# Kernel tuning notes

Measured on AMD Instinct MI355X. Metric: run time of the kernel, lower is better.

The kernel has to match this reference:

```python
import jax, jax.numpy as jnp
import numpy as np

ROPE_FREQ = 100.0

def _rope1d(tok, pos, freq):
    # tok: [B, H, N, D] (D even), pos: [B, N] int positions
    D = tok.shape[-1]
    inv_freq = 1.0 / (freq ** (jnp.arange(0, D, 2, dtype=jnp.float32) / D))  # [D/2]
    ang = pos[:, None, :, None].astype(jnp.float32) * inv_freq  # [B,1,N,D/2]
    cos = jnp.concatenate([jnp.cos(ang), jnp.cos(ang)], axis=-1).astype(tok.dtype)
    sin = jnp.concatenate([jnp.sin(ang), jnp.sin(ang)], axis=-1).astype(tok.dtype)
    x1, x2 = jnp.split(tok, 2, axis=-1)
    rot = jnp.concatenate([-x2, x1], axis=-1)  # rotate_half
    return tok * cos + rot * sin

def _rope2d(tok, pos2d, freq=ROPE_FREQ):
    # tok: [B, H, N, D]; first half of D encodes y (pos2d[...,0]), second half x (pos2d[...,1])
    y, x = jnp.split(tok, 2, axis=-1)
    y = _rope1d(y, pos2d[..., 0], freq)
    x = _rope1d(x, pos2d[..., 1], freq)
    return jnp.concatenate([y, x], axis=-1)

def setup_inputs() -> dict:
    key = jax.random.key(0)
    B, N, D, Hh = 2, 2048, 768, 12
    ks = jax.random.split(key, 8)
    x = jax.random.normal(ks[0], (B, N, D), dtype=jnp.float32)
    pos2d = jax.random.randint(ks[1], (B, N, 2), 0, 64)
    rope_mask = jax.random.randint(ks[2], (B, N), 0, 2).astype(jnp.bool_)
    s = 1.0 / np.sqrt(D)
    qkv_w = jax.random.normal(ks[3], (3 * D, D), dtype=jnp.float32) * s
    qkv_b = jnp.zeros((3 * D,), dtype=jnp.float32)
    proj_w = jax.random.normal(ks[4], (D, D), dtype=jnp.float32) * s
    proj_b = jnp.zeros((D,), dtype=jnp.float32)
    return {"x": x, "qkv_w": qkv_w, "qkv_b": qkv_b, "proj_w": proj_w,
            "proj_b": proj_b, "pos2d": pos2d, "rope_mask": rope_mask}

def reference(x, qkv_w, qkv_b, proj_w, proj_b, pos2d, rope_mask):
    B, N, C = x.shape
    num_heads = 12
    head_dim = C // num_heads
    scale = head_dim ** -0.5
    qkv = x @ qkv_w.T + qkv_b  # [B,N,3C]
    qkv = qkv.reshape(B, N, 3, num_heads, head_dim).transpose(2, 0, 3, 1, 4)
    q, k, v = qkv[0], qkv[1], qkv[2]  # each [B,H,N,hd]
    q_rope = _rope2d(q, pos2d)
    k_rope = _rope2d(k, pos2d)
    mask = rope_mask[:, None, :, None]  # [B,1,N,1]
    q = jnp.where(mask, q_rope, q)
    k = jnp.where(mask, k_rope, k)
    attn = jnp.einsum('bhqd,bhkd->bhqk', q, k) * scale
    attn = jax.nn.softmax(attn, axis=-1)
    out = jnp.einsum('bhqk,bhkd->bhqd', attn, v)
    out = out.transpose(0, 2, 1, 3).reshape(B, N, C)
    out = out @ proj_w.T + proj_b
    return out
```

## Files before the change

### kernel.cpp

```cpp
#include <hip/hip_runtime.h>
#include <stdint.h>

#define B_  2
#define N_  2048
#define C_  768
#define H_  12
#define NT  (B_*N_)
#define C3  (3*C_)

typedef _Float16 h8 __attribute__((ext_vector_type(8)));
typedef _Float16 h4 __attribute__((ext_vector_type(4)));
typedef float    f4 __attribute__((ext_vector_type(4)));
typedef float    f16x __attribute__((ext_vector_type(16)));
typedef uint32_t u4 __attribute__((ext_vector_type(4)));

__device__ __forceinline__ void gload16(const void* g, void* l) {
  __builtin_amdgcn_global_load_lds((const __attribute__((address_space(1))) void*)g,
                                   (__attribute__((address_space(3))) void*)l,
                                   16, 0, 0);
}

__device__ __forceinline__ int xcd_swz(int flat, int nwg) {
  return (flat & 7) * (nwg >> 3) + (flat >> 3);
}

__global__ __launch_bounds__(256) void cvt3(const float* __restrict__ x,
                                            const float* __restrict__ w1,
                                            const float* __restrict__ w2,
                                            _Float16* __restrict__ xo,
                                            _Float16* __restrict__ w1o,
                                            _Float16* __restrict__ w2o) {
  const int NX8  = NT*C_/8;
  const int NW18 = C3*C_/8;
  int c = blockIdx.x*256 + threadIdx.x;
  const float* s; _Float16* d; int off;
  if (c < NX8)            { s = x;  d = xo;  off = c; }
  else if (c < NX8+NW18)  { s = w1; d = w1o; off = c - NX8; }
  else                    { s = w2; d = w2o; off = c - NX8 - NW18; }
  f4 a = *(const f4*)(s + (size_t)off*8);
  f4 b = *(const f4*)(s + (size_t)off*8 + 4);
  h8 o;
#pragma unroll
  for (int j = 0; j < 4; ++j) { o[j] = (_Float16)a[j]; o[j+4] = (_Float16)b[j]; }
  *(h8*)(d + (size_t)off*8) = o;
}

template<int BM, int BN>
__global__ __launch_bounds__(256) void gemm_bt(const _Float16* __restrict__ A,
                                               const _Float16* __restrict__ W,
                                               const float* __restrict__ bias,
                                               _Float16* __restrict__ Ch,
                                               float* __restrict__ Cf,
                                               int M, int N, int K) {
  __shared__ _Float16 Alds[2][BM*32];
  __shared__ _Float16 Wlds[2][BN*32];
  const int tid = threadIdx.x, lane = tid & 63, w = tid >> 6;
  const int flat = blockIdx.y * gridDim.x + blockIdx.x;
  const int wid  = xcd_swz(flat, gridDim.x * gridDim.y);
  const int bx = wid % gridDim.x, by = wid / gridDim.x;
  const int m0 = by*BM, n0 = bx*BN;
  const int wm = w >> 1, wn = w & 1;
  const int fr = lane & 15, fq = lane >> 4;
  constexpr int MT = BM/32, NTt = BN/32;
  constexpr int AI = (BM*4)/256, WI = (BN*4)/256;

  f4 acc[MT][NTt] = {};

  const _Float16* Agp[AI];
  const _Float16* Wgp[WI];
#pragma unroll
  for (int i = 0; i < AI; ++i) { int c = i*256 + tid; Agp[i] = A + (size_t)(m0 + (c>>2))*K + (c&3)*8; }
#pragma unroll
  for (int i = 0; i < WI; ++i) { int c = i*256 + tid; Wgp[i] = W + (size_t)(n0 + (c>>2))*K + (c&3)*8; }

  auto GSTAGE = [&](int buf, int kk) {
#pragma unroll
    for (int i = 0; i < AI; ++i) gload16(Agp[i] + kk, &Alds[buf][(i*256 + w*64)*8]);
#pragma unroll
    for (int i = 0; i < WI; ++i) gload16(Wgp[i] + kk, &Wlds[buf][(i*256 + w*64)*8]);
  };

  GSTAGE(0, 0);
  int cur = 0;
  for (int kk = 0; kk < K; kk += 32) {
    __syncthreads();
    if (kk + 32 < K) GSTAGE(cur^1, kk + 32);
    h8 af[MT], wf[NTt];
#pragma unroll
    for (int mt = 0; mt < MT; ++mt)
      af[mt] = *(const h8*)&Alds[cur][(wm*(BM/2) + mt*16 + fr)*32 + fq*8];
#pragma unroll
    for (int nt = 0; nt < NTt; ++nt)
      wf[nt] = *(const h8*)&Wlds[cur][(wn*(BN/2) + nt*16 + fr)*32 + fq*8];
#pragma unroll
    for (int mt = 0; mt < MT; ++mt)
#pragma unroll
      for (int nt = 0; nt < NTt; ++nt)
        acc[mt][nt] = __builtin_amdgcn_mfma_f32_16x16x32_f16(af[mt], wf[nt], acc[mt][nt], 0, 0, 0);
    cur ^= 1;
  }

#pragma unroll
  for (int nt = 0; nt < NTt; ++nt) {
    const int col = n0 + wn*(BN/2) + nt*16 + fr;
    const float bv = bias[col];
#pragma unroll
    for (int mt = 0; mt < MT; ++mt) {
      const int row = m0 + wm*(BM/2) + mt*16 + fq*4;
#pragma unroll
      for (int j = 0; j < 4; ++j) {
        const float v = acc[mt][nt][j] + bv;
        if (Ch) Ch[(size_t)(row+j)*N + col] = (_Float16)v;
        else    Cf[(size_t)(row+j)*N + col] = v;
      }
    }
  }
}

__global__ __launch_bounds__(256) void rope_scatter(const _Float16* __restrict__ QKV,
                                                    const int* __restrict__ pos2d,
                                                    const void* __restrict__ maskraw,
                                                    _Float16* __restrict__ Q,
                                                    _Float16* __restrict__ Kd,
                                                    _Float16* __restrict__ Vt) {
  const int tid = threadIdx.x;
  __shared__ int sflags;
  if (tid == 0) sflags = 0;
  __syncthreads();
  const unsigned char* mbytes = (const unsigned char*)maskraw;
  int fl = 0;
#pragma unroll
  for (int k2 = 0; k2 < 16; ++k2) {
    unsigned char v = mbytes[tid*16 + k2];
    if (v == 0x3f) fl |= 1;
    if ((k2 & 3) && v) fl |= 2;
  }
  if (fl) atomicOr(&sflags, fl);
  __syncthreads();
  const int mode = (sflags & 1) ? 2 : ((sflags & 2) ? 1 : 0);

  const int g  = blockIdx.x*256 + tid;
  const int bh = g >> 11;
  const int n  = g & 2047;
  const int b  = bh / H_, h = bh % H_;
  const int t  = b*N_ + n;

  bool msk;
  if (mode == 1)      msk = mbytes[t] != 0;
  else if (mode == 0) msk = ((const int*)maskraw)[t] != 0;
  else                msk = ((const float*)maskraw)[t] != 0.0f;

  const float py = (float)pos2d[t*2 + 0];
  const float px = (float)pos2d[t*2 + 1];

  const float QS = 0.1803368801f;

  const _Float16* row = QKV + (size_t)t*C3 + h*64;
  h8 qv[8], kv[8], vv[8];
#pragma unroll
  for (int c = 0; c < 8; ++c) {
    qv[c] = *(const h8*)&row[c*8];
    kv[c] = *(const h8*)&row[C_   + c*8];
    vv[c] = *(const h8*)&row[2*C_ + c*8];
  }
  h8 qo[8], ko[8];
#pragma unroll
  for (int i = 0; i < 16; ++i) {
    const float invf = exp2f((float)i * -0.4152410118f);
    float sy, cy, sx, cx;
    __sincosf(py * invf, &sy, &cy);
    __sincosf(px * invf, &sx, &cx);
    {
      float a = (float)qv[i>>3][i&7], bq = (float)qv[(i+16)>>3][(i+16)&7];
      float r1 = msk ? (a*cy - bq*sy) : a;
      float r2 = msk ? (bq*cy + a*sy) : bq;
      qo[i>>3][i&7]           = (_Float16)(r1 * QS);
      qo[(i+16)>>3][(i+16)&7] = (_Float16)(r2 * QS);
      float ak = (float)kv[i>>3][i&7], bk = (float)kv[(i+16)>>3][(i+16)&7];
      float s1 = msk ? (ak*cy - bk*sy) : ak;
      float s2 = msk ? (bk*cy + ak*sy) : bk;
      ko[i>>3][i&7]           = (_Float16)s1;
      ko[(i+16)>>3][(i+16)&7] = (_Float16)s2;
    }
    {
      float a = (float)qv[(i+32)>>3][(i+32)&7], bq = (float)qv[(i+48)>>3][(i+48)&7];
      float r1 = msk ? (a*cx - bq*sx) : a;
      float r2 = msk ? (bq*cx + a*sx) : bq;
      qo[(i+32)>>3][(i+32)&7] = (_Float16)(r1 * QS);
      qo[(i+48)>>3][(i+48)&7] = (_Float16)(r2 * QS);
      float ak = (float)kv[(i+32)>>3][(i+32)&7], bk = (float)kv[(i+48)>>3][(i+48)&7];
      float s1 = msk ? (ak*cx - bk*sx) : ak;
      float s2 = msk ? (bk*cx + ak*sx) : bk;
      ko[(i+32)>>3][(i+32)&7] = (_Float16)s1;
      ko[(i+48)>>3][(i+48)&7] = (_Float16)s2;
    }
  }
  _Float16* Qrow = Q  + ((size_t)bh*N_ + n)*64;
  _Float16* Krow = Kd + ((size_t)bh*N_ + n)*64;
#pragma unroll
  for (int c = 0; c < 8; ++c) { *(h8*)&Qrow[c*8] = qo[c]; *(h8*)&Krow[c*8] = ko[c]; }
  _Float16* Vb = Vt + (size_t)bh*64*N_ + n;
#pragma unroll
  for (int d = 0; d < 64; ++d) Vb[(size_t)d*N_] = vv[d>>3][d&7];
}

#define KSPLIT 2
__global__ __launch_bounds__(256, 3) void attn(const _Float16* __restrict__ Q,
                                               const _Float16* __restrict__ K,
                                               const _Float16* __restrict__ Vt,
                                               _Float16* __restrict__ Opart,
                                               float* __restrict__ lpart) {
  __shared__ _Float16 Klds[2][64*64];
  __shared__ _Float16 Vlds[2][64*64];
  const int tid = threadIdx.x, lane = tid & 63, w = tid >> 6;
  const int q32 = lane & 31;
  const int hi  = lane >> 5;
  const int flat = blockIdx.x + gridDim.x*(blockIdx.y + gridDim.y*blockIdx.z);
  const int wid  = xcd_swz(flat, 16*24*KSPLIT);
  const int qi = wid & 15;
  const int bh = (wid >> 4) % 24;
  const int z  = wid / (16*24);
  const int q0 = qi * 128;
  const int kb0 = z * (N_/KSPLIT), kb1 = kb0 + N_/KSPLIT;
  const _Float16* Qb = Q  + (size_t)bh*N_*64;
  const _Float16* Kb = K  + (size_t)bh*N_*64;
  const _Float16* Vb = Vt + (size_t)bh*64*N_;

  h8 qf[4];
#pragma unroll
  for (int s = 0; s < 4; ++s)
    qf[s] = *(const h8*)&Qb[(size_t)(q0 + w*32 + q32)*64 + s*16 + hi*8];

  f16x o2[2][2];
#pragma unroll
  for (int par = 0; par < 2; ++par)
#pragma unroll
    for (int dg = 0; dg < 2; ++dg)
#pragma unroll
      for (int r = 0; r < 16; ++r) o2[par][dg][r] = 0.f;
  float l_r = 0.f;

  const int sr_l = lane >> 3;
  const int scsw = ((lane & 7) ^ sr_l) * 8;
#define STAGE(buf, kb)                                                          \
  {                                                                             \
    _Float16* kl = &Klds[buf][(w*64)*8];                                        \
    _Float16* vl = &Vlds[buf][(w*64)*8];                                        \
    int r0 = w*8 + sr_l;                                                        \
    gload16(Kb + (size_t)((kb) + r0)*64 + scsw,      kl);                       \
    gload16(Vb + (size_t)r0*N_ + (kb) + scsw,        vl);                       \
    gload16(Kb + (size_t)((kb) + 32 + r0)*64 + scsw, kl + 256*8);               \
    gload16(Vb + (size_t)(32 + r0)*N_ + (kb) + scsw, vl + 256*8);               \
  }

  STAGE(0, kb0);
  int cur = 0;
  const int xr = (q32 & 7) << 3;

  for (int kb = kb0; kb < kb1; kb += 64) {
    __syncthreads();
    if (kb + 64 < kb1) STAGE(cur^1, kb + 64);

#pragma unroll
    for (int kg = 0; kg < 2; ++kg) {
      f16x st;
#pragma unroll
      for (int r = 0; r < 16; ++r) st[r] = -8.65617025f;
      __builtin_amdgcn_s_setprio(1);
#pragma unroll
      for (int s = 0; s < 4; ++s) {
        h8 kf = *(const h8*)&Klds[cur][(kg*32 + q32)*64 + ((s*16 + hi*8) ^ xr)];
        st = __builtin_amdgcn_mfma_f32_32x32x16_f16(kf, qf[s], st, 0, 0, 0);
      }
      __builtin_amdgcn_s_setprio(0);
      float p[16];
      float lacc = 0.f;
#pragma unroll
      for (int r = 0; r < 16; ++r) {
        p[r] = __builtin_amdgcn_exp2f(st[r]);
        lacc += p[r];
      }
      l_r += lacc;
      uint32_t dd[8];
#pragma unroll
      for (int m = 0; m < 8; ++m)
        dd[m] = __builtin_bit_cast(uint32_t, __builtin_amdgcn_cvt_pkrtz(p[2*m], p[2*m+1]));
#pragma unroll
      for (int s16 = 0; s16 < 2; ++s16) {
        uint32_t e0 = dd[4*s16+0], e2 = dd[4*s16+2];
        asm("v_permlane32_swap_b32 %0, %1" : "+v"(e0), "+v"(e2));
        uint32_t e1 = dd[4*s16+1], e3 = dd[4*s16+3];
        asm("v_permlane32_swap_b32 %0, %1" : "+v"(e1), "+v"(e3));
        u4 bb;
        bb[0] = e0; bb[1] = e1; bb[2] = e2; bb[3] = e3;
        h8 pb = __builtin_bit_cast(h8, bb);
        const int kcol = kg*32 + s16*16 + hi*8;
        __builtin_amdgcn_s_setprio(1);
#pragma unroll
        for (int dg = 0; dg < 2; ++dg) {
          h8 vf = *(const h8*)&Vlds[cur][(dg*32 + q32)*64 + (kcol ^ xr)];
          o2[s16][dg] = __builtin_amdgcn_mfma_f32_32x32x16_f16(vf, pb, o2[s16][dg], 0, 0, 0);
        }
        __builtin_amdgcn_s_setprio(0);
      }
    }
    cur ^= 1;
  }

  l_r += __shfl_xor(l_r, 32);

  _Float16* Ob = Opart + ((size_t)z*24 + bh)*N_*64;
  float*    lb = lpart + ((size_t)z*24 + bh)*N_;
  const int n = q0 + w*32 + q32;
  if (hi == 0) lb[n] = l_r;
#pragma unroll
  for (int dg = 0; dg < 2; ++dg)
#pragma unroll
    for (int rq = 0; rq < 4; ++rq) {
      h4 ov;
#pragma unroll
      for (int j = 0; j < 4; ++j)
        ov[j] = (_Float16)(o2[0][dg][rq*4 + j] + o2[1][dg][rq*4 + j]);
      *(h4*)&Ob[(size_t)n*64 + dg*32 + rq*8 + hi*4] = ov;
    }
}

__global__ __launch_bounds__(256) void combine(const _Float16* __restrict__ Opart,
                                               const float* __restrict__ lpart,
                                               _Float16* __restrict__ AO) {
  const int g  = blockIdx.x*256 + threadIdx.x;
  const int d8 = g & 7;
  const int n  = (g >> 3) & 2047;
  const int bh = g >> 14;
  const int b = bh / H_, h = bh % H_;
  const size_t r  = ((size_t)bh*N_ + n);
  const size_t sp = (size_t)24*N_;
  f4 osum[2] = {};
  float l = 0.f;
#pragma unroll
  for (int z = 0; z < KSPLIT; ++z) {
    h8 oz = *(const h8*)&Opart[(r + z*sp)*64 + d8*8];
#pragma unroll
    for (int j = 0; j < 4; ++j) { osum[0][j] += (float)oz[j]; osum[1][j] += (float)oz[j+4]; }
    l += lpart[r + z*sp];
  }
  const float inv = 1.0f / l;
  h8 rr;
#pragma unroll
  for (int j = 0; j < 4; ++j) {
    rr[j]   = (_Float16)(osum[0][j] * inv);
    rr[j+4] = (_Float16)(osum[1][j] * inv);
  }
  *(h8*)&AO[((size_t)b*N_ + n)*C_ + h*64 + d8*8] = rr;
}

extern "C" void kernel_launch(void* const* d_in, const int* in_sizes, int n_in,
                              void* d_out, int out_size, void* d_ws, size_t ws_size,
                              hipStream_t stream) {
  (void)in_sizes; (void)n_in; (void)out_size; (void)ws_size;
  const float* x      = (const float*)d_in[0];
  const float* qkv_w  = (const float*)d_in[1];
  const float* qkv_b  = (const float*)d_in[2];
  const float* proj_w = (const float*)d_in[3];
  const float* proj_b = (const float*)d_in[4];
  const int*   pos2d  = (const int*)d_in[5];
  const void*  rmask  = d_in[6];
  float* out = (float*)d_out;
  char* ws = (char*)d_ws;

  _Float16* Wqh   = (_Float16*)(ws + 0);
  _Float16* Wph   = (_Float16*)(ws + 3538944);
  _Float16* Kh    = (_Float16*)(ws + 4718592);
  _Float16* Vth   = (_Float16*)(ws + 11010048);
  _Float16* Xh    = (_Float16*)(ws + 17301504);
  _Float16* QKVh  = (_Float16*)(ws + 23592960);
  _Float16* Qh    = Xh;
  _Float16* Opart = (_Float16*)(ws + 42467328);
  float*    lpart = (float*)(ws + 55050240);
  _Float16* AOh   = QKVh;

  cvt3<<<2688, 256, 0, stream>>>(x, qkv_w, proj_w, Xh, Wqh, Wph);
  gemm_bt<64,128><<<dim3(C3/128, NT/64), 256, 0, stream>>>(Xh, Wqh, qkv_b, QKVh, nullptr, NT, C3, C_);
  rope_scatter<<<(B_*H_*N_)/256, 256, 0, stream>>>(QKVh, pos2d, rmask, Qh, Kh, Vth);
  attn<<<dim3(N_/128, B_*H_, KSPLIT), 256, 0, stream>>>(Qh, Kh, Vth, Opart, lpart);
  combine<<<(24*N_*8)/256, 256, 0, stream>>>(Opart, lpart, AOh);
  gemm_bt<64,64><<<dim3(C_/64, NT/64), 256, 0, stream>>>(AOh, Wph, proj_b, nullptr, out, NT, C_, C_);
}
```

Baseline: 111.6 us.

## Fuse RoPE, scaling and Q/K/V scatter into the QKV GEMM epilogue

Adds a dedicated QKV GEMM whose epilogue applies bias, 2D RoPE (masked), the Q scale, and writes Q/K in head-major layout and V transposed, replacing the separate rope_scatter kernel. This removes a full write and re-read of the fp16 QKV intermediate plus one kernel launch. In exchange, the epilogue does scalar 2-byte scattered stores and strided V-transpose writes, recomputes sincos per tile, and adds mask-detection work to every GEMM block. The workspace layout is reshuffled so Q no longer aliases Xh.

```diff
diff --git a/kernel.cpp b/kernel.cpp
--- a/kernel.cpp
+++ b/kernel.cpp
@@ -43,6 +43,125 @@
 #pragma unroll
   for (int j = 0; j < 4; ++j) { o[j] = (_Float16)a[j]; o[j+4] = (_Float16)b[j]; }
   *(h8*)(d + (size_t)off*8) = o;
+}
+
+__global__ __launch_bounds__(256) void gemm_qkv(const _Float16* __restrict__ A,
+                                                const _Float16* __restrict__ W,
+                                                const float* __restrict__ bias,
+                                                const int* __restrict__ pos2d,
+                                                const void* __restrict__ maskraw,
+                                                _Float16* __restrict__ Qd,
+                                                _Float16* __restrict__ Kd,
+                                                _Float16* __restrict__ Vtd) {
+  constexpr int BM = 64, BN = 128, K = C_;
+  __shared__ _Float16 Alds[2][BM*32];
+  __shared__ _Float16 Wlds[2][BN*32];
+  __shared__ int sflags;
+  const int tid = threadIdx.x, lane = tid & 63, w = tid >> 6;
+
+  if (tid == 0) sflags = 0;
+  __syncthreads();
+  const unsigned char* mbytes = (const unsigned char*)maskraw;
+  int fl = 0;
+#pragma unroll
+  for (int k2 = 0; k2 < 16; ++k2) {
+    unsigned char v = mbytes[tid*16 + k2];
+    if (v == 0x3f) fl |= 1;
+    if ((k2 & 3) && v) fl |= 2;
+  }
+  if (fl) atomicOr(&sflags, fl);
+
+  const int flat = blockIdx.y * gridDim.x + blockIdx.x;
+  const int wid  = xcd_swz(flat, gridDim.x * gridDim.y);
+  const int bx = wid % gridDim.x, by = wid / gridDim.x;
+  const int m0 = by*BM, n0 = bx*BN;
+  const int wm = w >> 1, wn = w & 1;
+  const int fr = lane & 15, fq = lane >> 4;
+
+  f4 acc[2][4] = {};
+
+  const _Float16* Agp = A + (size_t)(m0 + (tid>>2))*K + (tid&3)*8;
+  const _Float16* Wgp0 = W + (size_t)(n0 + (tid>>2))*K + (tid&3)*8;
+  const _Float16* Wgp1 = W + (size_t)(n0 + 64 + (tid>>2))*K + (tid&3)*8;
+
+  auto GSTAGE = [&](int buf, int kk) {
+    gload16(Agp  + kk, &Alds[buf][(w*64)*8]);
+    gload16(Wgp0 + kk, &Wlds[buf][(w*64)*8]);
+    gload16(Wgp1 + kk, &Wlds[buf][(256 + w*64)*8]);
+  };
+
+  GSTAGE(0, 0);
+  int cur = 0;
+  for (int kk = 0; kk < K; kk += 32) {
+    __syncthreads();
+    if (kk + 32 < K) GSTAGE(cur^1, kk + 32);
+    h8 af[2], wf[4];
+#pragma unroll
+    for (int mt = 0; mt < 2; ++mt)
+      af[mt] = *(const h8*)&Alds[cur][(wm*32 + mt*16 + fr)*32 + fq*8];
+#pragma unroll
+    for (int nt = 0; nt < 4; ++nt)
+      wf[nt] = *(const h8*)&Wlds[cur][(wn*64 + nt*16 + fr)*32 + fq*8];
+#pragma unroll
+    for (int mt = 0; mt < 2; ++mt)
+#pragma unroll
+      for (int nt = 0; nt < 4; ++nt)
+        acc[mt][nt] = __builtin_amdgcn_mfma_f32_16x16x32_f16(af[mt], wf[nt], acc[mt][nt], 0, 0, 0);
+    cur ^= 1;
+  }
+
+  const int cb   = (n0 >> 6) + wn;
+  const int matc = cb / 12;
+  const int h    = cb % 12;
+  const int mode = (sflags & 1) ? 2 : ((sflags & 2) ? 1 : 0);
+  float bv[4];
+#pragma unroll
+  for (int nt = 0; nt < 4; ++nt) bv[nt] = bias[cb*64 + nt*16 + fr];
+
+  if (matc < 2) {
+    const float invf = exp2f((float)fr * -0.4152410118f);
+    const float sc = (matc == 0) ? 0.1803368801f : 1.0f;
+    _Float16* base = (matc == 0) ? Qd : Kd;
+#pragma unroll
+    for (int mt = 0; mt < 2; ++mt)
+#pragma unroll
+      for (int j = 0; j < 4; ++j) {
+        const int t = m0 + wm*32 + mt*16 + fq*4 + j;
+        const int b = t >> 11, n = t & 2047;
+        bool msk;
+        if (mode == 1)      msk = mbytes[t] != 0;
+        else if (mode == 0) msk = ((const int*)maskraw)[t] != 0;
+        else                msk = ((const float*)maskraw)[t] != 0.0f;
+        const float py = (float)pos2d[t*2 + 0];
+        const float px = (float)pos2d[t*2 + 1];
+        float sy, cy, sx, cx;
+        __sincosf(py * invf, &sy, &cy);
+        __sincosf(px * invf, &sx, &cx);
+        const float a0 = acc[mt][0][j] + bv[0], a1 = acc[mt][1][j] + bv[1];
+        const float a2 = acc[mt][2][j] + bv[2], a3 = acc[mt][3][j] + bv[3];
+        const float r0 = msk ? (a0*cy - a1*sy) : a0;
+        const float r1 = msk ? (a1*cy + a0*sy) : a1;
+        const float r2 = msk ? (a2*cx - a3*sx) : a2;
+        const float r3 = msk ? (a3*cx + a2*sx) : a3;
+        _Float16* dst = base + ((size_t)(b*H_ + h)*N_ + n)*64;
+        dst[fr]      = (_Float16)(r0 * sc);
+        dst[fr + 16] = (_Float16)(r1 * sc);
+        dst[fr + 32] = (_Float16)(r2 * sc);
+        dst[fr + 48] = (_Float16)(r3 * sc);
+      }
+  } else {
+#pragma unroll
+    for (int mt = 0; mt < 2; ++mt)
+#pragma unroll
+      for (int j = 0; j < 4; ++j) {
+        const int t = m0 + wm*32 + mt*16 + fq*4 + j;
+        const int b = t >> 11, n = t & 2047;
+        _Float16* vb = Vtd + (size_t)(b*H_ + h)*64*N_ + n;
+#pragma unroll
+        for (int nt = 0; nt < 4; ++nt)
+          vb[(size_t)(nt*16 + fr)*N_] = (_Float16)(acc[mt][nt][j] + bv[nt]);
+      }
+  }
 }
 
 template<int BM, int BN>
@@ -115,93 +234,6 @@
       }
     }
   }
-}
-
-__global__ __launch_bounds__(256) void rope_scatter(const _Float16* __restrict__ QKV,
-                                                    const int* __restrict__ pos2d,
-                                                    const void* __restrict__ maskraw,
-                                                    _Float16* __restrict__ Q,
-                                                    _Float16* __restrict__ Kd,
-                                                    _Float16* __restrict__ Vt) {
-  const int tid = threadIdx.x;
-  __shared__ int sflags;
-  if (tid == 0) sflags = 0;
-  __syncthreads();
-  const unsigned char* mbytes = (const unsigned char*)maskraw;
-  int fl = 0;
-#pragma unroll
-  for (int k2 = 0; k2 < 16; ++k2) {
-    unsigned char v = mbytes[tid*16 + k2];
-    if (v == 0x3f) fl |= 1;
-    if ((k2 & 3) && v) fl |= 2;
-  }
-  if (fl) atomicOr(&sflags, fl);
-  __syncthreads();
-  const int mode = (sflags & 1) ? 2 : ((sflags & 2) ? 1 : 0);
-
-  const int g  = blockIdx.x*256 + tid;
-  const int bh = g >> 11;
-  const int n  = g & 2047;
-  const int b  = bh / H_, h = bh % H_;
-  const int t  = b*N_ + n;
-
-  bool msk;
-  if (mode == 1)      msk = mbytes[t] != 0;
-  else if (mode == 0) msk = ((const int*)maskraw)[t] != 0;
-  else                msk = ((const float*)maskraw)[t] != 0.0f;
-
-  const float py = (float)pos2d[t*2 + 0];
-  const float px = (float)pos2d[t*2 + 1];
-
-  const float QS = 0.1803368801f;
-
-  const _Float16* row = QKV + (size_t)t*C3 + h*64;
-  h8 qv[8], kv[8], vv[8];
-#pragma unroll
-  for (int c = 0; c < 8; ++c) {
-    qv[c] = *(const h8*)&row[c*8];
-    kv[c] = *(const h8*)&row[C_   + c*8];
-    vv[c] = *(const h8*)&row[2*C_ + c*8];
-  }
-  h8 qo[8], ko[8];
-#pragma unroll
-  for (int i = 0; i < 16; ++i) {
-    const float invf = exp2f((float)i * -0.4152410118f);
-    float sy, cy, sx, cx;
-    __sincosf(py * invf, &sy, &cy);
-    __sincosf(px * invf, &sx, &cx);
-    {
-      float a = (float)qv[i>>3][i&7], bq = (float)qv[(i+16)>>3][(i+16)&7];
-      float r1 = msk ? (a*cy - bq*sy) : a;
-      float r2 = msk ? (bq*cy + a*sy) : bq;
-      qo[i>>3][i&7]           = (_Float16)(r1 * QS);
-      qo[(i+16)>>3][(i+16)&7] = (_Float16)(r2 * QS);
-      float ak = (float)kv[i>>3][i&7], bk = (float)kv[(i+16)>>3][(i+16)&7];
-      float s1 = msk ? (ak*cy - bk*sy) : ak;
-      float s2 = msk ? (bk*cy + ak*sy) : bk;
-      ko[i>>3][i&7]           = (_Float16)s1;
-      ko[(i+16)>>3][(i+16)&7] = (_Float16)s2;
-    }
-    {
-      float a = (float)qv[(i+32)>>3][(i+32)&7], bq = (float)qv[(i+48)>>3][(i+48)&7];
-      float r1 = msk ? (a*cx - bq*sx) : a;
-      float r2 = msk ? (bq*cx + a*sx) : bq;
-      qo[(i+32)>>3][(i+32)&7] = (_Float16)(r1 * QS);
-      qo[(i+48)>>3][(i+48)&7] = (_Float16)(r2 * QS);
-      float ak = (float)kv[(i+32)>>3][(i+32)&7], bk = (float)kv[(i+48)>>3][(i+48)&7];
-      float s1 = msk ? (ak*cx - bk*sx) : ak;
-      float s2 = msk ? (bk*cx + ak*sx) : bk;
-      ko[(i+32)>>3][(i+32)&7] = (_Float16)s1;
-      ko[(i+48)>>3][(i+48)&7] = (_Float16)s2;
-    }
-  }
-  _Float16* Qrow = Q  + ((size_t)bh*N_ + n)*64;
-  _Float16* Krow = Kd + ((size_t)bh*N_ + n)*64;
-#pragma unroll
-  for (int c = 0; c < 8; ++c) { *(h8*)&Qrow[c*8] = qo[c]; *(h8*)&Krow[c*8] = ko[c]; }
-  _Float16* Vb = Vt + (size_t)bh*64*N_ + n;
-#pragma unroll
-  for (int d = 0; d < 64; ++d) Vb[(size_t)d*N_] = vv[d>>3][d&7];
 }
 
 #define KSPLIT 2
@@ -373,15 +405,13 @@
   _Float16* Kh    = (_Float16*)(ws + 4718592);
   _Float16* Vth   = (_Float16*)(ws + 11010048);
   _Float16* Xh    = (_Float16*)(ws + 17301504);
-  _Float16* QKVh  = (_Float16*)(ws + 23592960);
-  _Float16* Qh    = Xh;
-  _Float16* Opart = (_Float16*)(ws + 42467328);
-  float*    lpart = (float*)(ws + 55050240);
-  _Float16* AOh   = QKVh;
+  _Float16* Qh    = (_Float16*)(ws + 23592960);
+  _Float16* Opart = (_Float16*)(ws + 29884416);
+  float*    lpart = (float*)(ws + 42467328);
+  _Float16* AOh   = (_Float16*)(ws + 43253760);
 
   cvt3<<<2688, 256, 0, stream>>>(x, qkv_w, proj_w, Xh, Wqh, Wph);
-  gemm_bt<64,128><<<dim3(C3/128, NT/64), 256, 0, stream>>>(Xh, Wqh, qkv_b, QKVh, nullptr, NT, C3, C_);
-  rope_scatter<<<(B_*H_*N_)/256, 256, 0, stream>>>(QKVh, pos2d, rmask, Qh, Kh, Vth);
+  gemm_qkv<<<dim3(C3/128, NT/64), 256, 0, stream>>>(Xh, Wqh, qkv_b, pos2d, rmask, Qh, Kh, Vth);
   attn<<<dim3(N_/128, B_*H_, KSPLIT), 256, 0, stream>>>(Qh, Kh, Vth, Opart, lpart);
   combine<<<(24*N_*8)/256, 256, 0, stream>>>(Opart, lpart, AOh);
   gemm_bt<64,64><<<dim3(C_/64, NT/64), 256, 0, stream>>>(AOh, Wph, proj_b, nullptr, out, NT, C_, C_);
```

Measured after the change: 101.9 us. 8.7% less time.
